# Kernel tuning notes

Measured on AMD Instinct MI355X. Metric: run time of the kernel, lower is better.

## Reference

```python
import jax, jax.numpy as jnp
import numpy as np

N_NODES = 100000
N_EDGES = 1200000
N_GRAPHS = 128
D = 64  # input_size == num_classes == 64


def setup_inputs() -> dict:
    key = jax.random.key(0)
    ks = jax.random.split(key, 8)
    feats = jax.random.normal(ks[0], (N_NODES, D), dtype=jnp.float32)
    src = jax.random.randint(ks[1], (N_EDGES,), 0, N_NODES, dtype=jnp.int64)
    dst = jax.random.randint(ks[2], (N_EDGES,), 0, N_NODES, dtype=jnp.int64)
    graph_id = jnp.sort(jax.random.randint(ks[3], (N_NODES,), 0, N_GRAPHS, dtype=jnp.int64))
    # Linear layer params (torch nn.Linear: y = x @ W.T + b); store as [in, out]
    s = 1.0 / np.sqrt(D)
    W1 = jax.random.uniform(ks[4], (D, D), jnp.float32, -s, s)
    b1 = jax.random.uniform(ks[5], (D,), jnp.float32, -s, s)
    W2 = jax.random.uniform(ks[6], (D, D), jnp.float32, -s, s)
    b2 = jax.random.uniform(ks[7], (D,), jnp.float32, -s, s)
    return {"feats": feats, "src": src, "dst": dst, "graph_id": graph_id,
            "W1": W1, "b1": b1, "W2": W2, "b2": b2}


def reference(feats, src, dst, graph_id, W1, b1, W2, b2):
    # GINConv (sum aggregator, eps=0): h = Linear(x + sum_{j in N(i)} x_j)
    agg1 = jax.ops.segment_sum(feats[src], dst, num_segments=N_NODES)
    h = jax.nn.relu((feats + agg1) @ W1 + b1)
    agg2 = jax.ops.segment_sum(h[src], dst, num_segments=N_NODES)
    h2 = (h + agg2) @ W2 + b2
    # SumPooling: per-graph sum of node features -> [N_GRAPHS, D]
    return jax.ops.segment_sum(h2, graph_id, num_segments=N_GRAPHS)
```

## Files before the change

### kernel.cpp

```cpp
#include <hip/hip_runtime.h>

#define D 64
#define NNODES 100000
#define NGRAPHS 128
#define NTILES ((NNODES + 15) / 16)
#define BUCKW 512
#define NBUCK ((NNODES + BUCKW - 1) / BUCKW)
#define EPB 4096

typedef unsigned int uint;
typedef unsigned short ushort;
typedef __attribute__((ext_vector_type(8))) short short8;
typedef __attribute__((ext_vector_type(4))) float f32x4;

__device__ __forceinline__ ushort f2b(float f) {
    uint u = __float_as_uint(f);
    uint r = (u + 0x7fffu + ((u >> 16) & 1u)) >> 16;
    return (ushort)r;
}
__device__ __forceinline__ float b2f(ushort h) {
    return __uint_as_float(((uint)h) << 16);
}

__global__ void zero_kernel(int* __restrict__ buf, int n4) {
    int i = blockIdx.x * blockDim.x + threadIdx.x;
    int stride = gridDim.x * blockDim.x;
    int4 z = make_int4(0, 0, 0, 0);
    for (; i < n4; i += stride) ((int4*)buf)[i] = z;
}

__global__ void cast_kernel(const float* __restrict__ in, ushort* __restrict__ outb, int n4) {
    int i = blockIdx.x * blockDim.x + threadIdx.x;
    int stride = gridDim.x * blockDim.x;
    for (; i < n4; i += stride) {
        float4 v = ((const float4*)in)[i];
        ushort4 o;
        o.x = f2b(v.x); o.y = f2b(v.y); o.z = f2b(v.z); o.w = f2b(v.w);
        ((ushort4*)outb)[i] = o;
    }
}

__global__ void prep_w_kernel(const float* __restrict__ W, ushort* __restrict__ Wswz) {
    int t = threadIdx.x;
    int j = t >> 6, lane = t & 63;
    int c = j >> 1, h = j & 1;
    int col = 16 * c + (lane & 15);
    int kbase = (lane >> 4) * 8 + 32 * h;
#pragma unroll
    for (int i = 0; i < 8; ++i)
        Wswz[(size_t)t * 8 + i] = f2b(W[(kbase + i) * D + col]);
}

__global__ void bhist_kernel(const int* __restrict__ dst, int* __restrict__ ghist,
                             int nE, int nblk) {
    __shared__ int lh[NBUCK];
    int t = threadIdx.x, blk = blockIdx.x;
    for (int i = t; i < NBUCK; i += 256) lh[i] = 0;
    __syncthreads();
    int base = blk * EPB + t * 16;
    if (base + 16 <= nE) {
#pragma unroll
        for (int j = 0; j < 4; ++j) {
            int4 d = *(const int4*)(dst + base + j * 4);
            atomicAdd(&lh[d.x >> 9], 1);
            atomicAdd(&lh[d.y >> 9], 1);
            atomicAdd(&lh[d.z >> 9], 1);
            atomicAdd(&lh[d.w >> 9], 1);
        }
    } else {
        int lim = min(base + 16, nE);
        for (int e = base; e < lim; ++e) atomicAdd(&lh[dst[e] >> 9], 1);
    }
    __syncthreads();
    for (int i = t; i < NBUCK; i += 256) ghist[(size_t)i * nblk + blk] = lh[i];
}

__global__ void gpartial_kernel(const int* __restrict__ g, int* __restrict__ gsum, int M) {
    __shared__ int sh[256];
    int t = threadIdx.x;
    int base = (blockIdx.x * 256 + t) * 4;
    int s = 0;
    if (base + 4 <= M) {
        int4 v = *(const int4*)(g + base);
        s = v.x + v.y + v.z + v.w;
    } else {
        for (int i = base; i < M; ++i) s += g[i];
    }
    sh[t] = s;
    __syncthreads();
    for (int d = 128; d > 0; d >>= 1) {
        if (t < d) sh[t] += sh[t + d];
        __syncthreads();
    }
    if (t == 0) gsum[blockIdx.x] = sh[0];
}

__global__ void gscanb_kernel(const int* __restrict__ gsum, int* __restrict__ gbase2,
                              int* __restrict__ bbase, int* __restrict__ off,
                              int nb, int nE) {
    __shared__ int sh[256];
    int t = threadIdx.x;
    sh[t] = (t < nb) ? gsum[t] : 0;
    __syncthreads();
    for (int d = 1; d < 256; d <<= 1) {
        int u = (t >= d) ? sh[t - d] : 0;
        __syncthreads();
        sh[t] += u;
        __syncthreads();
    }
    if (t < nb) gbase2[t] = (t == 0) ? 0 : sh[t - 1];
    if (t == 0) {
        bbase[NBUCK] = nE;
        off[NNODES] = nE;
    }
}

__global__ void goffsets_kernel(int* __restrict__ g, const int* __restrict__ gbase2,
                                int* __restrict__ bbase, int M, int nblk) {
    __shared__ int sh[256];
    int t = threadIdx.x;
    int base = (blockIdx.x * 256 + t) * 4;
    int v0 = 0, v1 = 0, v2 = 0, v3 = 0;
    if (base + 4 <= M) {
        int4 v = *(const int4*)(g + base);
        v0 = v.x; v1 = v.y; v2 = v.z; v3 = v.w;
    } else {
        if (base < M)     v0 = g[base];
        if (base + 1 < M) v1 = g[base + 1];
        if (base + 2 < M) v2 = g[base + 2];
        if (base + 3 < M) v3 = g[base + 3];
    }
    int s = v0 + v1 + v2 + v3;
    sh[t] = s;
    __syncthreads();
    for (int d = 1; d < 256; d <<= 1) {
        int u = (t >= d) ? sh[t - d] : 0;
        __syncthreads();
        sh[t] += u;
        __syncthreads();
    }
    int e0 = gbase2[blockIdx.x] + sh[t] - s;
    int e1 = e0 + v0, e2 = e1 + v1, e3 = e2 + v2;
    if (base + 4 <= M) {
        *(int4*)(g + base) = make_int4(e0, e1, e2, e3);
    } else {
        if (base < M)     g[base]     = e0;
        if (base + 1 < M) g[base + 1] = e1;
        if (base + 2 < M) g[base + 2] = e2;
        if (base + 3 < M) g[base + 3] = e3;
    }
    int ev[4] = {e0, e1, e2, e3};
#pragma unroll
    for (int j = 0; j < 4; ++j) {
        int i = base + j;
        if (i < M && i % nblk == 0) bbase[i / nblk] = ev[j];
    }
}

__global__ void bscatter_kernel(const int* __restrict__ src, const int* __restrict__ dst,
                                const int* __restrict__ gbase, int* __restrict__ packed,
                                int nE, int nblk) {
    __shared__ int lcur[NBUCK];
    int t = threadIdx.x, blk = blockIdx.x;
    for (int i = t; i < NBUCK; i += 256) lcur[i] = gbase[(size_t)i * nblk + blk];
    __syncthreads();
    int base = blk * EPB + t * 16;
    if (base + 16 <= nE) {
#pragma unroll
        for (int j = 0; j < 4; ++j) {
            int4 d = *(const int4*)(dst + base + j * 4);
            int4 s4 = *(const int4*)(src + base + j * 4);
            int p0 = atomicAdd(&lcur[d.x >> 9], 1);
            int p1 = atomicAdd(&lcur[d.y >> 9], 1);
            int p2 = atomicAdd(&lcur[d.z >> 9], 1);
            int p3 = atomicAdd(&lcur[d.w >> 9], 1);
            packed[p0] = (s4.x << 9) | (d.x & 511);
            packed[p1] = (s4.y << 9) | (d.y & 511);
            packed[p2] = (s4.z << 9) | (d.z & 511);
            packed[p3] = (s4.w << 9) | (d.w & 511);
        }
    } else {
        int lim = min(base + 16, nE);
        for (int e = base; e < lim; ++e) {
            int p = atomicAdd(&lcur[dst[e] >> 9], 1);
            packed[p] = (src[e] << 9) | (dst[e] & 511);
        }
    }
}

__global__ void csr_build_kernel(const int* __restrict__ packed, const int* __restrict__ bbase,
                                 int* __restrict__ off, int* __restrict__ esrc) {
    __shared__ int lcnt[BUCKW];
    __shared__ int lcur[BUCKW];
    __shared__ int part[256];
    int t = threadIdx.x;
    int blk = blockIdx.x;
    int ebeg = bbase[blk], eend = bbase[blk + 1];
    lcnt[t] = 0; lcnt[t + 256] = 0;
    __syncthreads();
    for (int e = ebeg + t; e < eend; e += 256)
        atomicAdd(&lcnt[packed[e] & 511], 1);
    __syncthreads();
    int a = lcnt[2 * t], bv = lcnt[2 * t + 1];
    part[t] = a + bv;
    __syncthreads();
    for (int d = 1; d < 256; d <<= 1) {
        int u = (t >= d) ? part[t - d] : 0;
        __syncthreads();
        part[t] += u;
        __syncthreads();
    }
    int excl2 = (t == 0) ? 0 : part[t - 1];
    lcur[2 * t] = excl2;
    lcur[2 * t + 1] = excl2 + a;
    int node0 = blk * BUCKW + 2 * t;
    if (node0 < NNODES)     off[node0]     = ebeg + excl2;
    if (node0 + 1 < NNODES) off[node0 + 1] = ebeg + excl2 + a;
    __syncthreads();
    for (int e = ebeg + t; e < eend; e += 256) {
        int p = packed[e];
        int pos = ebeg + atomicAdd(&lcur[p & 511], 1);
        esrc[pos] = p >> 9;
    }
}

__device__ __forceinline__ float gather_row_b(const ushort* __restrict__ x,
                                              const int* __restrict__ esrc,
                                              int beg, int end, int lane, float acc) {
    int i = beg;
    while (i + 8 <= end) {
        int s0 = esrc[i + 0], s1 = esrc[i + 1], s2 = esrc[i + 2], s3 = esrc[i + 3];
        int s4 = esrc[i + 4], s5 = esrc[i + 5], s6 = esrc[i + 6], s7 = esrc[i + 7];
        ushort v0 = x[(size_t)s0 * D + lane], v1 = x[(size_t)s1 * D + lane];
        ushort v2 = x[(size_t)s2 * D + lane], v3 = x[(size_t)s3 * D + lane];
        ushort v4 = x[(size_t)s4 * D + lane], v5 = x[(size_t)s5 * D + lane];
        ushort v6 = x[(size_t)s6 * D + lane], v7 = x[(size_t)s7 * D + lane];
        acc += ((b2f(v0) + b2f(v1)) + (b2f(v2) + b2f(v3))) +
               ((b2f(v4) + b2f(v5)) + (b2f(v6) + b2f(v7)));
        i += 8;
    }
    if (i + 4 <= end) {
        int s0 = esrc[i + 0], s1 = esrc[i + 1], s2 = esrc[i + 2], s3 = esrc[i + 3];
        ushort v0 = x[(size_t)s0 * D + lane], v1 = x[(size_t)s1 * D + lane];
        ushort v2 = x[(size_t)s2 * D + lane], v3 = x[(size_t)s3 * D + lane];
        acc += (b2f(v0) + b2f(v1)) + (b2f(v2) + b2f(v3));
        i += 4;
    }
    for (; i < end; ++i) acc += b2f(x[(size_t)esrc[i] * D + lane]);
    return acc;
}

__global__ void gather_gemm1_kernel(const ushort* __restrict__ xb,
                                    const int* __restrict__ off,
                                    const int* __restrict__ esrc,
                                    const ushort* __restrict__ Wswz,
                                    const float* __restrict__ b1,
                                    ushort* __restrict__ hb, int ntiles) {
    int tid = threadIdx.x;
    int w = tid >> 6, lane = tid & 63;
    int tile = blockIdx.x * 4 + w;
    if (tile >= ntiles) return;

    short8 bfrag[8];
#pragma unroll
    for (int j = 0; j < 8; ++j)
        bfrag[j] = *(const short8*)(Wswz + ((size_t)j * 64 + lane) * 8);

    int r = lane & 15, h = lane >> 4;
    int rbase = tile * 16;
    int node = rbase + r;

    float accA[8], accB[8];
    {
        const ushort* p = xb + (size_t)node * D + h * 8;
        short8 sA = *(const short8*)(p);
        short8 sB = *(const short8*)(p + 32);
#pragma unroll
        for (int q = 0; q < 8; ++q) {
            accA[q] = b2f((ushort)sA[q]);
            accB[q] = b2f((ushort)sB[q]);
        }
    }

    int beg = off[node], end = off[node + 1];
    int i = beg;
    for (; i + 4 <= end; i += 4) {
        int e0 = esrc[i], e1 = esrc[i + 1], e2 = esrc[i + 2], e3 = esrc[i + 3];
        const ushort* p0 = xb + (size_t)e0 * D + h * 8;
        const ushort* p1 = xb + (size_t)e1 * D + h * 8;
        const ushort* p2 = xb + (size_t)e2 * D + h * 8;
        const ushort* p3 = xb + (size_t)e3 * D + h * 8;
        short8 v0A = *(const short8*)(p0), v0B = *(const short8*)(p0 + 32);
        short8 v1A = *(const short8*)(p1), v1B = *(const short8*)(p1 + 32);
        short8 v2A = *(const short8*)(p2), v2B = *(const short8*)(p2 + 32);
        short8 v3A = *(const short8*)(p3), v3B = *(const short8*)(p3 + 32);
#pragma unroll
        for (int q = 0; q < 8; ++q) {
            accA[q] += (b2f((ushort)v0A[q]) + b2f((ushort)v1A[q]))
                     + (b2f((ushort)v2A[q]) + b2f((ushort)v3A[q]));
            accB[q] += (b2f((ushort)v0B[q]) + b2f((ushort)v1B[q]))
                     + (b2f((ushort)v2B[q]) + b2f((ushort)v3B[q]));
        }
    }
    for (; i < end; ++i) {
        const ushort* p = xb + (size_t)esrc[i] * D + h * 8;
        short8 vA = *(const short8*)(p), vB = *(const short8*)(p + 32);
#pragma unroll
        for (int q = 0; q < 8; ++q) {
            accA[q] += b2f((ushort)vA[q]);
            accB[q] += b2f((ushort)vB[q]);
        }
    }

    short8 a0, a1;
#pragma unroll
    for (int q = 0; q < 8; ++q) {
        a0[q] = (short)f2b(accA[q]);
        a1[q] = (short)f2b(accB[q]);
    }

    f32x4 acc0 = {0.f, 0.f, 0.f, 0.f};
    f32x4 acc1 = {0.f, 0.f, 0.f, 0.f};
    f32x4 acc2 = {0.f, 0.f, 0.f, 0.f};
    f32x4 acc3 = {0.f, 0.f, 0.f, 0.f};
    acc0 = __builtin_amdgcn_mfma_f32_16x16x32_bf16(a0, bfrag[0], acc0, 0, 0, 0);
    acc0 = __builtin_amdgcn_mfma_f32_16x16x32_bf16(a1, bfrag[1], acc0, 0, 0, 0);
    acc1 = __builtin_amdgcn_mfma_f32_16x16x32_bf16(a0, bfrag[2], acc1, 0, 0, 0);
    acc1 = __builtin_amdgcn_mfma_f32_16x16x32_bf16(a1, bfrag[3], acc1, 0, 0, 0);
    acc2 = __builtin_amdgcn_mfma_f32_16x16x32_bf16(a0, bfrag[4], acc2, 0, 0, 0);
    acc2 = __builtin_amdgcn_mfma_f32_16x16x32_bf16(a1, bfrag[5], acc2, 0, 0, 0);
    acc3 = __builtin_amdgcn_mfma_f32_16x16x32_bf16(a0, bfrag[6], acc3, 0, 0, 0);
    acc3 = __builtin_amdgcn_mfma_f32_16x16x32_bf16(a1, bfrag[7], acc3, 0, 0, 0);

    int colb = lane & 15;
    int rowb = (lane >> 4) * 4;
#pragma unroll
    for (int rr = 0; rr < 4; ++rr) {
        size_t rowoff = (size_t)(rbase + rowb + rr) * D;
        hb[rowoff + colb +  0] = f2b(fmaxf(acc0[rr] + b1[colb +  0], 0.f));
        hb[rowoff + colb + 16] = f2b(fmaxf(acc1[rr] + b1[colb + 16], 0.f));
        hb[rowoff + colb + 32] = f2b(fmaxf(acc2[rr] + b1[colb + 32], 0.f));
        hb[rowoff + colb + 48] = f2b(fmaxf(acc3[rr] + b1[colb + 48], 0.f));
    }
}

__global__ void gather_pool_kernel(const ushort* __restrict__ hb,
                                   const int* __restrict__ off,
                                   const int* __restrict__ esrc,
                                   const int* __restrict__ gid,
                                   float* __restrict__ P,
                                   float* __restrict__ cntg, int n) {
    int tid = threadIdx.x;
    int w = tid >> 6, lane = tid & 63;
    int waves_total = gridDim.x * 4;
    int wave_id = blockIdx.x * 4 + w;
    int chunk = (n + waves_total - 1) / waves_total;
    int start = wave_id * chunk;
    int end = min(start + chunk, n);

    float accp = 0.f;
    int cur = -1, cc = 0;
    for (int node = start; node < end; ++node) {
        float acc = b2f(hb[(size_t)node * D + lane]);
        acc = gather_row_b(hb, esrc, off[node], off[node + 1], lane, acc);
        int g = gid[node];
        if (g != cur) {
            if (cur >= 0) {
                atomicAdd(&P[cur * D + lane], accp);
                if (lane == 0) atomicAdd(&cntg[cur], (float)cc);
            }
            cur = g; accp = 0.f; cc = 0;
        }
        accp += acc;
        cc++;
    }
    if (cur >= 0) {
        atomicAdd(&P[cur * D + lane], accp);
        if (lane == 0) atomicAdd(&cntg[cur], (float)cc);
    }
}

__global__ void final_kernel(const float* __restrict__ P,
                             const float* __restrict__ cntg,
                             const float* __restrict__ W2,
                             const float* __restrict__ b2,
                             float* __restrict__ out) {
    __shared__ float Ws[D * D];
    __shared__ float bs[D];
    __shared__ float xs[4][D];
    int tid = threadIdx.x;
    for (int i = tid; i < D * D / 4; i += blockDim.x)
        ((float4*)Ws)[i] = ((const float4*)W2)[i];
    if (tid < D) bs[tid] = b2[tid];
    __syncthreads();

    int w = tid >> 6, lane = tid & 63;
    int g = blockIdx.x * 4 + w;
    if (g >= NGRAPHS) return;
    xs[w][lane] = P[g * D + lane];
    float acc = cntg[g] * bs[lane];
#pragma unroll
    for (int k = 0; k < D; ++k)
        acc = fmaf(xs[w][k], Ws[k * D + lane], acc);
    out[g * D + lane] = acc;
}

extern "C" void kernel_launch(void* const* d_in, const int* in_sizes, int n_in,
                              void* d_out, int out_size, void* d_ws, size_t ws_size,
                              hipStream_t stream) {
    const float* feats = (const float*)d_in[0];
    const int*   src   = (const int*)d_in[1];
    const int*   dst   = (const int*)d_in[2];
    const int*   gid   = (const int*)d_in[3];
    const float* W1    = (const float*)d_in[4];
    const float* b1    = (const float*)d_in[5];
    const float* W2    = (const float*)d_in[6];
    const float* b2    = (const float*)d_in[7];
    float* out = (float*)d_out;

    int nE = in_sizes[1];
    int nblk = (nE + EPB - 1) / EPB;
    int M = NBUCK * nblk;
    int gb = (M + 1023) / 1024;

    int*    bbase  = (int*)d_ws;
    int*    gsum   = bbase + 256;
    int*    gbase2 = gsum + 256;
    float*  P      = (float*)(gbase2 + 256);
    float*  cntg   = P + NGRAPHS * D;
    int*    off    = (int*)(cntg + 128);
    int*    ghist  = off + ((NNODES + 7) & ~3);
    int*    packed = ghist + ((M + 3) & ~3);
    int*    esrc   = packed + ((nE + 3) & ~3);
    ushort* Wswz   = (ushort*)(esrc + ((nE + 3) & ~3));
    ushort* xb     = Wswz + 4096;
    ushort* hb     = xb + (size_t)NNODES * D;

    bhist_kernel<<<nblk, 256, 0, stream>>>(dst, ghist, nE, nblk);
    gpartial_kernel<<<gb, 256, 0, stream>>>(ghist, gsum, M);
    gscanb_kernel<<<1, 256, 0, stream>>>(gsum, gbase2, bbase, off, gb, nE);
    goffsets_kernel<<<gb, 256, 0, stream>>>(ghist, gbase2, bbase, M, nblk);
    bscatter_kernel<<<nblk, 256, 0, stream>>>(src, dst, ghist, packed, nE, nblk);
    csr_build_kernel<<<NBUCK, 256, 0, stream>>>(packed, bbase, off, esrc);

    cast_kernel<<<2048, 256, 0, stream>>>(feats, xb, NNODES * D / 4);
    prep_w_kernel<<<1, 512, 0, stream>>>(W1, Wswz);
    zero_kernel<<<8, 256, 0, stream>>>((int*)P, (NGRAPHS * D + 128) / 4);

    gather_gemm1_kernel<<<(NTILES + 3) / 4, 256, 0, stream>>>(xb, off, esrc, Wswz, b1, hb, NTILES);

    gather_pool_kernel<<<2048, 256, 0, stream>>>(hb, off, esrc, gid, P, cntg, NNODES);
    final_kernel<<<NGRAPHS / 4, 256, 0, stream>>>(P, cntg, W2, b2, out);
}
```

Baseline: 165.1 us.

## Split pooling into node self-pass and edge-parallel gather with per-edge graph ids

Replaces the node-parallel neighbor gather in the pooling stage with two kernels: a light self-term pooling pass and an edge-parallel pass that streams CSR-ordered edges with a precomputed per-edge graph id. The CSR build now writes egid alongside esrc, using graph ids staged in shared memory. The aim is to remove load imbalance and per-node offset lookups, and to let the edge kernel issue vectorized index loads with 16 gathers in flight. In exchange it writes and reads an extra 4.8MB egid array and adds a kernel launch.

```diff
diff --git a/kernel.cpp b/kernel.cpp
--- a/kernel.cpp
+++ b/kernel.cpp
@@ -189,14 +189,20 @@
 }
 
 __global__ void csr_build_kernel(const int* __restrict__ packed, const int* __restrict__ bbase,
-                                 int* __restrict__ off, int* __restrict__ esrc) {
+                                 const int* __restrict__ gid,
+                                 int* __restrict__ off, int* __restrict__ esrc,
+                                 int* __restrict__ egid) {
     __shared__ int lcnt[BUCKW];
     __shared__ int lcur[BUCKW];
+    __shared__ int lgid[BUCKW];
     __shared__ int part[256];
     int t = threadIdx.x;
     int blk = blockIdx.x;
     int ebeg = bbase[blk], eend = bbase[blk + 1];
     lcnt[t] = 0; lcnt[t + 256] = 0;
+    int n0 = blk * BUCKW + t, n1 = blk * BUCKW + t + 256;
+    lgid[t]       = (n0 < NNODES) ? gid[n0] : 0;
+    lgid[t + 256] = (n1 < NNODES) ? gid[n1] : 0;
     __syncthreads();
     for (int e = ebeg + t; e < eend; e += 256)
         atomicAdd(&lcnt[packed[e] & 511], 1);
@@ -219,35 +225,11 @@
     __syncthreads();
     for (int e = ebeg + t; e < eend; e += 256) {
         int p = packed[e];
-        int pos = ebeg + atomicAdd(&lcur[p & 511], 1);
+        int loc = p & 511;
+        int pos = ebeg + atomicAdd(&lcur[loc], 1);
         esrc[pos] = p >> 9;
-    }
-}
-
-__device__ __forceinline__ float gather_row_b(const ushort* __restrict__ x,
-                                              const int* __restrict__ esrc,
-                                              int beg, int end, int lane, float acc) {
-    int i = beg;
-    while (i + 8 <= end) {
-        int s0 = esrc[i + 0], s1 = esrc[i + 1], s2 = esrc[i + 2], s3 = esrc[i + 3];
-        int s4 = esrc[i + 4], s5 = esrc[i + 5], s6 = esrc[i + 6], s7 = esrc[i + 7];
-        ushort v0 = x[(size_t)s0 * D + lane], v1 = x[(size_t)s1 * D + lane];
-        ushort v2 = x[(size_t)s2 * D + lane], v3 = x[(size_t)s3 * D + lane];
-        ushort v4 = x[(size_t)s4 * D + lane], v5 = x[(size_t)s5 * D + lane];
-        ushort v6 = x[(size_t)s6 * D + lane], v7 = x[(size_t)s7 * D + lane];
-        acc += ((b2f(v0) + b2f(v1)) + (b2f(v2) + b2f(v3))) +
-               ((b2f(v4) + b2f(v5)) + (b2f(v6) + b2f(v7)));
-        i += 8;
-    }
-    if (i + 4 <= end) {
-        int s0 = esrc[i + 0], s1 = esrc[i + 1], s2 = esrc[i + 2], s3 = esrc[i + 3];
-        ushort v0 = x[(size_t)s0 * D + lane], v1 = x[(size_t)s1 * D + lane];
-        ushort v2 = x[(size_t)s2 * D + lane], v3 = x[(size_t)s3 * D + lane];
-        acc += (b2f(v0) + b2f(v1)) + (b2f(v2) + b2f(v3));
-        i += 4;
-    }
-    for (; i < end; ++i) acc += b2f(x[(size_t)esrc[i] * D + lane]);
-    return acc;
+        egid[pos] = lgid[loc];
+    }
 }
 
 __global__ void gather_gemm1_kernel(const ushort* __restrict__ xb,
@@ -344,12 +326,10 @@
     }
 }
 
-__global__ void gather_pool_kernel(const ushort* __restrict__ hb,
-                                   const int* __restrict__ off,
-                                   const int* __restrict__ esrc,
-                                   const int* __restrict__ gid,
-                                   float* __restrict__ P,
-                                   float* __restrict__ cntg, int n) {
+__global__ void pool_self_kernel(const ushort* __restrict__ hb,
+                                 const int* __restrict__ gid,
+                                 float* __restrict__ P,
+                                 float* __restrict__ cntg, int n) {
     int tid = threadIdx.x;
     int w = tid >> 6, lane = tid & 63;
     int waves_total = gridDim.x * 4;
@@ -361,8 +341,7 @@
     float accp = 0.f;
     int cur = -1, cc = 0;
     for (int node = start; node < end; ++node) {
-        float acc = b2f(hb[(size_t)node * D + lane]);
-        acc = gather_row_b(hb, esrc, off[node], off[node + 1], lane, acc);
+        float v = b2f(hb[(size_t)node * D + lane]);
         int g = gid[node];
         if (g != cur) {
             if (cur >= 0) {
@@ -371,13 +350,87 @@
             }
             cur = g; accp = 0.f; cc = 0;
         }
-        accp += acc;
+        accp += v;
         cc++;
     }
     if (cur >= 0) {
         atomicAdd(&P[cur * D + lane], accp);
         if (lane == 0) atomicAdd(&cntg[cur], (float)cc);
     }
+}
+
+__global__ void edge_pool_kernel(const ushort* __restrict__ hb,
+                                 const int* __restrict__ esrc,
+                                 const int* __restrict__ egid,
+                                 float* __restrict__ P, int nE) {
+    int tid = threadIdx.x;
+    int w = tid >> 6, lane = tid & 63;
+    int waves_total = gridDim.x * 4;
+    int wave_id = blockIdx.x * 4 + w;
+    int chunk = ((nE + waves_total - 1) / waves_total + 15) & ~15;
+    int start = wave_id * chunk;
+    int end = min(start + chunk, nE);
+    if (start >= nE) return;
+
+    float accp = 0.f;
+    int cur = -1;
+    int i = start;
+    for (; i + 16 <= end; i += 16) {
+        int4 s0 = *(const int4*)(esrc + i);
+        int4 s1 = *(const int4*)(esrc + i + 4);
+        int4 s2 = *(const int4*)(esrc + i + 8);
+        int4 s3 = *(const int4*)(esrc + i + 12);
+        int4 g0 = *(const int4*)(egid + i);
+        int4 g1 = *(const int4*)(egid + i + 4);
+        int4 g2 = *(const int4*)(egid + i + 8);
+        int4 g3 = *(const int4*)(egid + i + 12);
+        ushort v0  = hb[(size_t)s0.x * D + lane];
+        ushort v1  = hb[(size_t)s0.y * D + lane];
+        ushort v2  = hb[(size_t)s0.z * D + lane];
+        ushort v3  = hb[(size_t)s0.w * D + lane];
+        ushort v4  = hb[(size_t)s1.x * D + lane];
+        ushort v5  = hb[(size_t)s1.y * D + lane];
+        ushort v6  = hb[(size_t)s1.z * D + lane];
+        ushort v7  = hb[(size_t)s1.w * D + lane];
+        ushort v8  = hb[(size_t)s2.x * D + lane];
+        ushort v9  = hb[(size_t)s2.y * D + lane];
+        ushort v10 = hb[(size_t)s2.z * D + lane];
+        ushort v11 = hb[(size_t)s2.w * D + lane];
+        ushort v12 = hb[(size_t)s3.x * D + lane];
+        ushort v13 = hb[(size_t)s3.y * D + lane];
+        ushort v14 = hb[(size_t)s3.z * D + lane];
+        ushort v15 = hb[(size_t)s3.w * D + lane];
+        int gg[16] = {g0.x, g0.y, g0.z, g0.w, g1.x, g1.y, g1.z, g1.w,
+                      g2.x, g2.y, g2.z, g2.w, g3.x, g3.y, g3.z, g3.w};
+        ushort vv[16] = {v0, v1, v2, v3, v4, v5, v6, v7,
+                         v8, v9, v10, v11, v12, v13, v14, v15};
+        if (gg[0] == cur && gg[15] == cur) {
+            float s = ((b2f(vv[0]) + b2f(vv[1])) + (b2f(vv[2]) + b2f(vv[3])))
+                    + ((b2f(vv[4]) + b2f(vv[5])) + (b2f(vv[6]) + b2f(vv[7])))
+                    + ((b2f(vv[8]) + b2f(vv[9])) + (b2f(vv[10]) + b2f(vv[11])))
+                    + ((b2f(vv[12]) + b2f(vv[13])) + (b2f(vv[14]) + b2f(vv[15])));
+            accp += s;
+        } else {
+#pragma unroll
+            for (int q = 0; q < 16; ++q) {
+                if (gg[q] != cur) {
+                    if (cur >= 0) atomicAdd(&P[cur * D + lane], accp);
+                    cur = gg[q]; accp = 0.f;
+                }
+                accp += b2f(vv[q]);
+            }
+        }
+    }
+    for (; i < end; ++i) {
+        int g = egid[i];
+        ushort v = hb[(size_t)esrc[i] * D + lane];
+        if (g != cur) {
+            if (cur >= 0) atomicAdd(&P[cur * D + lane], accp);
+            cur = g; accp = 0.f;
+        }
+        accp += b2f(v);
+    }
+    if (cur >= 0) atomicAdd(&P[cur * D + lane], accp);
 }
 
 __global__ void final_kernel(const float* __restrict__ P,
@@ -432,7 +485,8 @@
     int*    ghist  = off + ((NNODES + 7) & ~3);
     int*    packed = ghist + ((M + 3) & ~3);
     int*    esrc   = packed + ((nE + 3) & ~3);
-    ushort* Wswz   = (ushort*)(esrc + ((nE + 3) & ~3));
+    int*    egid   = esrc + ((nE + 3) & ~3);
+    ushort* Wswz   = (ushort*)(egid + ((nE + 3) & ~3));
     ushort* xb     = Wswz + 4096;
     ushort* hb     = xb + (size_t)NNODES * D;
 
@@ -441,7 +495,7 @@
     gscanb_kernel<<<1, 256, 0, stream>>>(gsum, gbase2, bbase, off, gb, nE);
     goffsets_kernel<<<gb, 256, 0, stream>>>(ghist, gbase2, bbase, M, nblk);
     bscatter_kernel<<<nblk, 256, 0, stream>>>(src, dst, ghist, packed, nE, nblk);
-    csr_build_kernel<<<NBUCK, 256, 0, stream>>>(packed, bbase, off, esrc);
+    csr_build_kernel<<<NBUCK, 256, 0, stream>>>(packed, bbase, gid, off, esrc, egid);
 
     cast_kernel<<<2048, 256, 0, stream>>>(feats, xb, NNODES * D / 4);
     prep_w_kernel<<<1, 512, 0, stream>>>(W1, Wswz);
@@ -449,6 +503,7 @@
 
     gather_gemm1_kernel<<<(NTILES + 3) / 4, 256, 0, stream>>>(xb, off, esrc, Wswz, b1, hb, NTILES);
 
-    gather_pool_kernel<<<2048, 256, 0, stream>>>(hb, off, esrc, gid, P, cntg, NNODES);
+    pool_self_kernel<<<512, 256, 0, stream>>>(hb, gid, P, cntg, NNODES);
+    edge_pool_kernel<<<2048, 256, 0, stream>>>(hb, esrc, egid, P, nE);
     final_kernel<<<NGRAPHS / 4, 256, 0, stream>>>(P, cntg, W2, b2, out);
 }
```

Result: no change. 164.8 us (-0.2%).
